# Performance work log

Measured on AMD Instinct MI355X. Metric: run time of the kernel, lower is better.

The kernel has to match this reference:

```python
import jax, jax.numpy as jnp
import numpy as np

N = 50000      # nodes
E = 800000     # edges
FIN = 128      # num_feature
EDIM = 16      # edge_dim
OUT = 64       # out_dim (per-head channels; concat=False averages heads)
H = 4          # heads
SCALE = 1.0 / float(np.sqrt(OUT))


def _layernorm(h, g, b):
    mu = h.mean(-1, keepdims=True)
    var = ((h - mu) ** 2).mean(-1, keepdims=True)
    return (h - mu) * jax.lax.rsqrt(var + 1e-5) * g + b


def _tconv(x, src, dst, ea, Wq, bq, Wk, bk, Wv, bv, We, Ws, bs):
    # PyG TransformerConv, concat=False, root_weight=True, eval mode (no dropout)
    n = x.shape[0]
    q = (x @ Wq + bq).reshape(n, H, OUT)[dst]   # [E,H,D] query at destination
    k = (x @ Wk + bk).reshape(n, H, OUT)[src]   # [E,H,D] key at source
    v = (x @ Wv + bv).reshape(n, H, OUT)[src]   # [E,H,D] value at source
    e = (ea @ We).reshape(-1, H, OUT)           # [E,H,D] edge embedding (no bias)
    logits = jnp.einsum('ehd,ehd->eh', q, k + e) * SCALE   # [E,H]
    # segment softmax over incoming edges of each destination node
    m = jax.lax.stop_gradient(jax.ops.segment_max(logits, dst, num_segments=n))
    a = jnp.exp(logits - m[dst])
    s = jax.ops.segment_sum(a, dst, num_segments=n)
    alpha = a / s[dst]                                     # [E,H]
    agg = jax.ops.segment_sum((v + e) * alpha[..., None], dst, num_segments=n)  # [N,H,D]
    return agg.mean(axis=1) + x @ Ws + bs      # concat=False -> head mean; + skip


def _forward(x, src, dst, ea, p1, p2, p3, g, b):
    h = x
    for p in (p1, p2, p3):
        h = jax.nn.gelu(_layernorm(_tconv(h, src, dst, ea, *p), g, b), approximate=False)
    return h


def setup_inputs() -> dict:
    key = jax.random.key(0)
    ks = iter(jax.random.split(key, 64))
    def nrm(shp, s=0.05):
        return jax.random.normal(next(ks), shp, jnp.float32) * s
    inp = {
        'x': nrm((N, FIN), 1.0),
        'edge_index': jax.random.randint(next(ks), (2, E), 0, N),
        'edge_attr': nrm((E, EDIM), 1.0),
    }
    for l, fin in ((1, FIN), (2, OUT), (3, OUT)):
        inp[f'Wq{l}'] = nrm((fin, H * OUT)); inp[f'bq{l}'] = jnp.zeros((H * OUT,), jnp.float32)
        inp[f'Wk{l}'] = nrm((fin, H * OUT)); inp[f'bk{l}'] = jnp.zeros((H * OUT,), jnp.float32)
        inp[f'Wv{l}'] = nrm((fin, H * OUT)); inp[f'bv{l}'] = jnp.zeros((H * OUT,), jnp.float32)
        inp[f'We{l}'] = nrm((EDIM, H * OUT))
        inp[f'Ws{l}'] = nrm((fin, OUT)); inp[f'bs{l}'] = jnp.zeros((OUT,), jnp.float32)
    inp['ln_g'] = jnp.ones((OUT,), jnp.float32)
    inp['ln_b'] = jnp.zeros((OUT,), jnp.float32)
    return inp


def reference(x, edge_index, edge_attr,
              Wq1, bq1, Wk1, bk1, Wv1, bv1, We1, Ws1, bs1,
              Wq2, bq2, Wk2, bk2, Wv2, bv2, We2, Ws2, bs2,
              Wq3, bq3, Wk3, bk3, Wv3, bv3, We3, Ws3, bs3,
              ln_g, ln_b):
    src, dst = edge_index[0], edge_index[1]
    p1 = (Wq1, bq1, Wk1, bk1, Wv1, bv1, We1, Ws1, bs1)
    p2 = (Wq2, bq2, Wk2, bk2, Wv2, bv2, We2, Ws2, bs2)
    p3 = (Wq3, bq3, Wk3, bk3, Wv3, bv3, We3, Ws3, bs3)
    return _forward(x, src, dst, edge_attr, p1, p2, p3, ln_g, ln_b)
```

## Files before the change

### kernel.cpp

```cpp
#include <hip/hip_runtime.h>
#include <hip/hip_bf16.h>
#include <math.h>

#define NNODES 50000
#define NEDGES 800000
#define HD     256
#define CW     448
#define NTOT   896
#define QS     0.18033688011112042f

typedef __hip_bfloat16 bf16;
typedef unsigned short u16;
typedef unsigned char  u8;
typedef unsigned int   u32;
typedef unsigned long long u64;
typedef __attribute__((ext_vector_type(8))) short bf16x8;
typedef __attribute__((ext_vector_type(4))) float f32x4;
typedef __attribute__((ext_vector_type(2))) float f32x2;

__device__ __forceinline__ float lo16f(u32 u) { return __uint_as_float(u << 16); }
__device__ __forceinline__ float hi16f(u32 u) { return __uint_as_float(u & 0xFFFF0000u); }
__device__ __forceinline__ short f2s(float v) { __hip_bfloat16 h = __float2bfloat16(v); return *(short*)&h; }

template<int CTRL>
__device__ __forceinline__ float dppadd(float x) {
    int t = __builtin_amdgcn_update_dpp(0, __float_as_int(x), CTRL, 0xF, 0xF, true);
    return x + __int_as_float(t);
}

__global__ void hist_kernel(const int* __restrict__ dst, int* __restrict__ deg, int E) {
    int e = blockIdx.x * 256 + threadIdx.x;
    if (e < E) atomicAdd(&deg[dst[e]], 1);
}

__global__ void scanA(const int* __restrict__ deg, int* __restrict__ locincl,
                      int* __restrict__ blocksum, int n) {
    int tid = threadIdx.x;
    int i = blockIdx.x * 256 + tid;
    int v = (i < n) ? deg[i] : 0;
    int lane = tid & 63, w = tid >> 6;
    int s = v;
    #pragma unroll
    for (int off = 1; off < 64; off <<= 1) {
        int t = __shfl_up(s, off);
        if (lane >= off) s += t;
    }
    __shared__ int wsum[4];
    if (lane == 63) wsum[w] = s;
    __syncthreads();
    for (int ww = 0; ww < w; ww++) s += wsum[ww];
    if (i < n) locincl[i] = s;
    if (tid == 255) blocksum[blockIdx.x] = s;
}

__global__ void scanB(const int* __restrict__ blocksum, int* __restrict__ blockoff,
                      int nb, int* __restrict__ rowptr, int n) {
    int tid = threadIdx.x;
    int v = (tid < nb) ? blocksum[tid] : 0;
    int lane = tid & 63, w = tid >> 6;
    int s = v;
    #pragma unroll
    for (int off = 1; off < 64; off <<= 1) {
        int t = __shfl_up(s, off);
        if (lane >= off) s += t;
    }
    __shared__ int wsum[4];
    if (lane == 63) wsum[w] = s;
    __syncthreads();
    for (int ww = 0; ww < w; ww++) s += wsum[ww];
    if (tid < nb) blockoff[tid] = s - v;
    if (tid == 255) rowptr[n] = s;
}

__global__ void scanC(const int* __restrict__ deg, const int* __restrict__ locincl,
                      const int* __restrict__ blockoff,
                      int* __restrict__ rowptr, int* __restrict__ cursor, int n) {
    int i = blockIdx.x * 256 + threadIdx.x;
    if (i < n) {
        int ex = locincl[i] - deg[i] + blockoff[blockIdx.x];
        rowptr[i] = ex;
        cursor[i] = ex;
    }
}

__global__ void scatter_kernel(const int* __restrict__ src, const int* __restrict__ dst,
                               int* __restrict__ cursor, int2* __restrict__ csr2, int E) {
    int e = blockIdx.x * 256 + threadIdx.x;
    if (e < E) {
        int d = dst[e];
        int p = atomicAdd(&cursor[d], 1);
        csr2[p] = make_int2(src[e], e);
    }
}

__global__ void pack_all(const float* __restrict__ Wq, const float* __restrict__ bq,
                         const float* __restrict__ Wk, const float* __restrict__ bk,
                         const float* __restrict__ Wv, const float* __restrict__ bv,
                         const float* __restrict__ We,
                         const float* __restrict__ Ws, const float* __restrict__ bs,
                         bf16* __restrict__ Wc, float* __restrict__ b, int K) {
    int n = blockIdx.x, c = threadIdx.x;
    float v, bb;
    if (n < 256)      { v = Wq[(size_t)c * 256 + n] * QS;    bb = bq[n] * QS; }
    else if (n < 320) {
        int t = n - 256, h = t >> 4, j = t & 15;
        float s = 0.f, sb = 0.f;
        #pragma unroll 8
        for (int d = 0; d < 64; d++) {
            float wv = We[j * HD + h * 64 + d];
            s += Wq[(size_t)c * 256 + h * 64 + d] * wv;
            sb += bq[h * 64 + d] * wv;
        }
        v = s * QS; bb = sb * QS;
    }
    else if (n < 384) { v = Ws[(size_t)c * 64  + (n - 320)]; bb = bs[n - 320]; }
    else if (n < 640) { v = Wv[(size_t)c * 256 + (n - 384)]; bb = bv[n - 384]; }
    else              { v = Wk[(size_t)c * 256 + (n - 640)]; bb = bk[n - 640]; }
    Wc[(size_t)n * K + c] = __float2bfloat16(v);
    if (c == 0) b[n] = bb;
}

template<typename TA, int K>
__global__ void __launch_bounds__(256) gemm_fused(
    const TA* __restrict__ A, const bf16* __restrict__ Wc, const float* __restrict__ bias,
    bf16* __restrict__ comb, bf16* __restrict__ vbuf, u8* __restrict__ k8)
{
    constexpr int KS  = K / 32;
    constexpr int CPR = K / 8;
    constexpr int SLD = CPR / 4;
    __shared__ short Bl[64 * K];
    __shared__ u8    Tr[64 * 128];
    int tid = threadIdx.x, w = tid >> 6, lane = tid & 63;
    int cl = lane & 15, aq = lane >> 4;
    int m0 = blockIdx.x * 64;
    int m  = m0 + w * 16 + cl;
    int rowc = (m < NNODES) ? m : (NNODES - 1);

    bf16x8 af[KS];
    if constexpr (sizeof(TA) == 4) {
        const float* ar = (const float*)A + (size_t)rowc * K;
        #pragma unroll
        for (int ks = 0; ks < KS; ks++) {
            const float4* ap = (const float4*)(ar + ks * 32 + aq * 8);
            float4 f0 = ap[0], f1 = ap[1];
            union { short s[8]; bf16x8 v; } t;
            t.s[0] = f2s(f0.x); t.s[1] = f2s(f0.y); t.s[2] = f2s(f0.z); t.s[3] = f2s(f0.w);
            t.s[4] = f2s(f1.x); t.s[5] = f2s(f1.y); t.s[6] = f2s(f1.z); t.s[7] = f2s(f1.w);
            af[ks] = t.v;
        }
    } else {
        const u16* ar = (const u16*)A + (size_t)rowc * K;
        #pragma unroll
        for (int ks = 0; ks < KS; ks++) af[ks] = *(const bf16x8*)(ar + ks * 32 + aq * 8);
    }

    uint4 sreg[SLD];
    auto SLOAD = [&](int chunk) {
        #pragma unroll
        for (int p = 0; p < SLD; p++) {
            int slot = tid + p * 256;
            int row = slot / CPR, j = slot % CPR;
            sreg[p] = *(const uint4*)((const u16*)Wc + (size_t)(chunk * 64 + row) * K + (j << 3));
        }
    };
    SLOAD(0);

    for (int chunk = 0; chunk < 14; chunk++) {
        __syncthreads();
        #pragma unroll
        for (int p = 0; p < SLD; p++) {
            int slot = tid + p * 256;
            int row = slot / CPR, j = slot % CPR;
            *(uint4*)&Bl[row * K + ((j ^ (row & 7)) << 3)] = sreg[p];
        }
        if (chunk < 13) SLOAD(chunk + 1);
        __syncthreads();

        f32x4 acc[4] = {};
        #pragma unroll
        for (int t = 0; t < 4; t++) {
            #pragma unroll
            for (int ks = 0; ks < KS; ks++) {
                int g = ((ks * 4 + aq) ^ (cl & 7)) << 3;
                bf16x8 bfr = *(const bf16x8*)&Bl[(t * 16 + cl) * K + g];
                acc[t] = __builtin_amdgcn_mfma_f32_16x16x32_bf16(bfr, af[ks], acc[t], 0, 0, 0);
            }
        }

        int r = w * 16 + cl;
        if (chunk < 10) {
            #pragma unroll
            for (int t = 0; t < 4; t++) {
                float4 bv = *(const float4*)&bias[chunk * 64 + t * 16 + aq * 4];
                u32 lo = (u32)(u16)f2s(acc[t][0] + bv.x) | ((u32)(u16)f2s(acc[t][1] + bv.y) << 16);
                u32 hi = (u32)(u16)f2s(acc[t][2] + bv.z) | ((u32)(u16)f2s(acc[t][3] + bv.w) << 16);
                *(uint2*)&Tr[r * 128 + (((t * 4 + aq) ^ (r & 15)) << 3)] = make_uint2(lo, hi);
            }
        } else {
            #pragma unroll
            for (int t = 0; t < 4; t++) {
                float4 bv = *(const float4*)&bias[chunk * 64 + t * 16 + aq * 4];
                u32 pk = __builtin_amdgcn_cvt_pk_fp8_f32(acc[t][0] + bv.x, acc[t][1] + bv.y, 0, false);
                pk = __builtin_amdgcn_cvt_pk_fp8_f32(acc[t][2] + bv.z, acc[t][3] + bv.w, pk, true);
                *(u32*)&Tr[r * 64 + (((t * 4 + aq) ^ (r & 15)) << 2)] = pk;
            }
        }
        __syncthreads();

        int r2 = tid >> 2, q = tid & 3;
        int gr = m0 + r2;
        if (gr < NNODES) {
            if (chunk < 10) {
                union { u32 d[4]; uint4 v; } o0, o1;
                #pragma unroll
                for (int j = 0; j < 4; j++) {
                    int g = ((q * 4 + j) ^ (r2 & 15)) << 3;
                    uint2 dv = *(const uint2*)&Tr[r2 * 128 + g];
                    if (j < 2) { o0.d[2 * j] = dv.x; o0.d[2 * j + 1] = dv.y; }
                    else       { o1.d[2 * (j - 2)] = dv.x; o1.d[2 * (j - 2) + 1] = dv.y; }
                }
                char* dst;
                if (chunk < 6) dst = (char*)comb + (size_t)gr * (CW * 2) + chunk * 128;
                else           dst = (char*)vbuf + (size_t)gr * 512 + (chunk - 6) * 128;
                *(uint4*)(dst + q * 32)      = o0.v;
                *(uint4*)(dst + q * 32 + 16) = o1.v;
            } else {
                union { u32 d[4]; uint4 v; } o;
                #pragma unroll
                for (int j = 0; j < 4; j++) {
                    int g = ((q * 4 + j) ^ (r2 & 15)) << 2;
                    o.d[j] = *(const u32*)&Tr[r2 * 64 + g];
                }
                *(uint4*)((char*)k8 + (size_t)gr * 256 + (chunk - 10) * 64 + q * 16) = o.v;
            }
        }
    }
}

__global__ void __launch_bounds__(256) node_fused(
    const int* __restrict__ rowptr, const int2* __restrict__ csr2,
    const float* __restrict__ eattr, const u16* __restrict__ comb,
    const u16* __restrict__ vbuf, const u8* __restrict__ k8,
    const float* __restrict__ We, const float* __restrict__ lng, const float* __restrict__ lnb,
    bf16* __restrict__ outB, float* __restrict__ outF)
{
    int tid = threadIdx.x, w = tid >> 6, lane = tid & 63;
    int n = blockIdx.x * 4 + w;
    int hg = lane >> 4, j16 = lane & 15, coff = 4 * lane;
    __shared__ float sAV[4][256];
    __shared__ float sAE[4][64];

    const u16* crow = comb + (size_t)n * CW;
    uint2 qv = *(const uint2*)(crow + coff);
    float qf0 = lo16f(qv.x), qf1 = hi16f(qv.x), qf2 = lo16f(qv.y), qf3 = hi16f(qv.y);
    float qwe_r = __uint_as_float((u32)crow[256 + lane] << 16);

    int e0 = __builtin_amdgcn_readfirstlane(rowptr[n]);
    int e1 = __builtin_amdgcn_readfirstlane(rowptr[n + 1]);

    float ss = 0.f, av0 = 0.f, av1 = 0.f, av2 = 0.f, av3 = 0.f, ae = 0.f;
    u32 vo = (u32)coff * 2u;
    u32 eo = (u32)j16 * 4u;

    auto EDGE = [&](int2 me) {
        u32 s = (u32)me.x, eid = (u32)me.y;
        u32   kw = *(const u32*)  ((const char*)k8    + ((s << 8) + (u32)coff));
        uint2 vw = *(const uint2*)((const char*)vbuf  + ((s << 9) + vo));
        float ea = *(const float*)((const char*)eattr + ((eid << 6) + eo));
        f32x2 k01 = __builtin_amdgcn_cvt_pk_f32_fp8(kw, false);
        f32x2 k23 = __builtin_amdgcn_cvt_pk_f32_fp8(kw, true);
        float part = qf0 * k01[0] + qf1 * k01[1] + qf2 * k23[0] + qf3 * k23[1] + qwe_r * ea;
        part = dppadd<0xB1>(part);
        part = dppadd<0x4E>(part);
        part = dppadd<0x141>(part);
        part = dppadd<0x140>(part);
        float alpha = __builtin_amdgcn_exp2f(part);
        ss += alpha;
        ae += alpha * ea;
        av0 += alpha * lo16f(vw.x); av1 += alpha * hi16f(vw.x);
        av2 += alpha * lo16f(vw.y); av3 += alpha * hi16f(vw.y);
    };

    int i = e0;
    int2 c0 = make_int2(0, 0), c1 = c0, c2 = c0, c3 = c0;
    if (i + 3 < e1) { c0 = csr2[i]; c1 = csr2[i + 1]; c2 = csr2[i + 2]; c3 = csr2[i + 3]; }
    for (; i + 7 < e1; i += 4) {
        int2 p0 = csr2[i + 4], p1 = csr2[i + 5], p2 = csr2[i + 6], p3 = csr2[i + 7];
        EDGE(c0); EDGE(c1); EDGE(c2); EDGE(c3);
        c0 = p0; c1 = p1; c2 = p2; c3 = p3;
    }
    if (i + 3 < e1) { EDGE(c0); EDGE(c1); EDGE(c2); EDGE(c3); i += 4; }
    for (; i < e1; ++i) { int2 cc = csr2[i]; EDGE(cc); }

    float inv = (ss > 0.f) ? 1.f / ss : 0.f;
    *(float4*)&sAV[w][coff] = make_float4(av0 * inv, av1 * inv, av2 * inv, av3 * inv);
    sAE[w][lane] = ae * inv;

    int d = lane;
    float val = 0.f;
    #pragma unroll
    for (int h = 0; h < 4; h++) {
        float xv = sAV[w][h * 64 + d];
        #pragma unroll
        for (int j = 0; j < 16; j++) xv += sAE[w][h * 16 + j] * We[j * HD + h * 64 + d];
        val += xv;
    }
    val = val * 0.25f + __uint_as_float((u32)crow[320 + d] << 16);

    float m = val;
    #pragma unroll
    for (int off = 1; off < 64; off <<= 1) m += __shfl_xor(m, off);
    m *= (1.f / 64.f);
    float diff = val - m;
    float vr = diff * diff;
    #pragma unroll
    for (int off = 1; off < 64; off <<= 1) vr += __shfl_xor(vr, off);
    vr *= (1.f / 64.f);
    float y = diff * rsqrtf(vr + 1e-5f) * lng[d] + lnb[d];
    float ge = 0.5f * y * (1.f + erff(y * 0.70710678118654752f));
    if (outF) outF[(size_t)n * 64 + d] = ge;
    else      outB[(size_t)n * 64 + d] = __float2bfloat16(ge);
}

extern "C" void kernel_launch(void* const* d_in, const int* in_sizes, int n_in,
                              void* d_out, int out_size, void* d_ws, size_t ws_size,
                              hipStream_t stream)
{
    const float* x     = (const float*)d_in[0];
    const int*   eidx  = (const int*)d_in[1];
    const float* eattr = (const float*)d_in[2];
    struct P { const float *Wq,*bq,*Wk,*bk,*Wv,*bv,*We,*Ws,*bs; };
    P p[3];
    for (int l = 0; l < 3; l++) {
        int base = 3 + l * 9;
        p[l].Wq = (const float*)d_in[base + 0]; p[l].bq = (const float*)d_in[base + 1];
        p[l].Wk = (const float*)d_in[base + 2]; p[l].bk = (const float*)d_in[base + 3];
        p[l].Wv = (const float*)d_in[base + 4]; p[l].bv = (const float*)d_in[base + 5];
        p[l].We = (const float*)d_in[base + 6];
        p[l].Ws = (const float*)d_in[base + 7]; p[l].bs = (const float*)d_in[base + 8];
    }
    const float* lng = (const float*)d_in[30];
    const float* lnb = (const float*)d_in[31];

    char* ws = (char*)d_ws;
    size_t off = 0;
    auto alloc = [&](size_t bytes) { void* pp = ws + off; off += (bytes + 255) & ~(size_t)255; return pp; };
    int*   rowptr   = (int*)  alloc((NNODES + 1) * 4);
    int*   cursor   = (int*)  alloc(NNODES * 4);
    int*   deg      = (int*)  alloc(NNODES * 4);
    int*   blocksum = (int*)  alloc(256 * 4);
    int*   blockoff = (int*)  alloc(256 * 4);
    int2*  csr2     = (int2*) alloc((size_t)NEDGES * 8);
    bf16*  hbuf     = (bf16*) alloc((size_t)NNODES * 64 * 2);
    bf16*  comb     = (bf16*) alloc((size_t)NNODES * CW * 2);
    bf16*  vbuf     = (bf16*) alloc((size_t)NNODES * 256 * 2);
    u8*    k8       = (u8*)   alloc((size_t)NNODES * 256);
    bf16*  Wc       = (bf16*) alloc((size_t)NTOT * 128 * 2);
    float* b896     = (float*)alloc(NTOT * 4);
    (void)ws_size;

    const int* srcArr = eidx;
    const int* dstArr = eidx + NEDGES;

    int NB = (NNODES + 255) / 256;
    (void)hipMemsetAsync(deg, 0, NNODES * 4, stream);
    hist_kernel<<<(NEDGES + 255) / 256, 256, 0, stream>>>(dstArr, deg, NEDGES);
    scanA<<<NB, 256, 0, stream>>>(deg, cursor, blocksum, NNODES);
    scanB<<<1, 256, 0, stream>>>(blocksum, blockoff, NB, rowptr, NNODES);
    scanC<<<NB, 256, 0, stream>>>(deg, cursor, blockoff, rowptr, cursor, NNODES);
    scatter_kernel<<<(NEDGES + 255) / 256, 256, 0, stream>>>(srcArr, dstArr, cursor, csr2, NEDGES);

    int gm = (NNODES + 63) / 64;
    int fins[3] = {128, 64, 64};

    const void* hin = x;
    for (int l = 0; l < 3; l++) {
        int FIN = fins[l];
        pack_all<<<NTOT, FIN, 0, stream>>>(p[l].Wq, p[l].bq, p[l].Wk, p[l].bk,
                                           p[l].Wv, p[l].bv, p[l].We, p[l].Ws, p[l].bs,
                                           Wc, b896, FIN);
        if (l == 0) gemm_fused<float, 128><<<gm, 256, 0, stream>>>((const float*)hin, Wc, b896, comb, vbuf, k8);
        else        gemm_fused<bf16,  64><<<gm, 256, 0, stream>>>((const bf16*)hin,  Wc, b896, comb, vbuf, k8);
        node_fused<<<NNODES / 4, 256, 0, stream>>>(rowptr, csr2, eattr, (const u16*)comb,
            (const u16*)vbuf, k8, p[l].We, lng, lnb,
            (l == 2) ? nullptr : hbuf, (l == 2) ? (float*)d_out : nullptr);
        hin = hbuf;
    }
}
```

Baseline: 733.4 us.

## Drop LDS staging in projection GEMM, split chunks over grid, scalarize edge addresses

The projection GEMM no longer stages weight tiles and output tiles through shared memory with barriers. Each wave now reads its B fragments straight from global memory (cache-resident weights) and writes results directly to the output buffers. The 14 output chunks are split across a second grid dimension to double the number of blocks, and the comb row stride shrinks from 448 to 384. In the edge loop, source and edge ids are made wave-uniform via readfirstlane so address arithmetic can stay scalar. The trade-off is fewer barriers and less LDS traffic against narrower, less coalesced global stores and repeated weight reads from cache.

```diff
diff --git a/kernel.cpp b/kernel.cpp
--- a/kernel.cpp
+++ b/kernel.cpp
@@ -5,7 +5,7 @@
 #define NNODES 50000
 #define NEDGES 800000
 #define HD     256
-#define CW     448
+#define CW     384
 #define NTOT   896
 #define QS     0.18033688011112042f
 
@@ -125,16 +125,12 @@
     const TA* __restrict__ A, const bf16* __restrict__ Wc, const float* __restrict__ bias,
     bf16* __restrict__ comb, bf16* __restrict__ vbuf, u8* __restrict__ k8)
 {
-    constexpr int KS  = K / 32;
-    constexpr int CPR = K / 8;
-    constexpr int SLD = CPR / 4;
-    __shared__ short Bl[64 * K];
-    __shared__ u8    Tr[64 * 128];
+    constexpr int KS = K / 32;
     int tid = threadIdx.x, w = tid >> 6, lane = tid & 63;
     int cl = lane & 15, aq = lane >> 4;
-    int m0 = blockIdx.x * 64;
-    int m  = m0 + w * 16 + cl;
+    int m = blockIdx.x * 64 + w * 16 + cl;
     int rowc = (m < NNODES) ? m : (NNODES - 1);
+    int cbeg = blockIdx.y * 7;
 
     bf16x8 af[KS];
     if constexpr (sizeof(TA) == 4) {
@@ -154,84 +150,38 @@
         for (int ks = 0; ks < KS; ks++) af[ks] = *(const bf16x8*)(ar + ks * 32 + aq * 8);
     }
 
-    uint4 sreg[SLD];
-    auto SLOAD = [&](int chunk) {
-        #pragma unroll
-        for (int p = 0; p < SLD; p++) {
-            int slot = tid + p * 256;
-            int row = slot / CPR, j = slot % CPR;
-            sreg[p] = *(const uint4*)((const u16*)Wc + (size_t)(chunk * 64 + row) * K + (j << 3));
-        }
-    };
-    SLOAD(0);
-
-    for (int chunk = 0; chunk < 14; chunk++) {
-        __syncthreads();
-        #pragma unroll
-        for (int p = 0; p < SLD; p++) {
-            int slot = tid + p * 256;
-            int row = slot / CPR, j = slot % CPR;
-            *(uint4*)&Bl[row * K + ((j ^ (row & 7)) << 3)] = sreg[p];
-        }
-        if (chunk < 13) SLOAD(chunk + 1);
-        __syncthreads();
-
+    for (int ci = 0; ci < 7; ci++) {
+        int chunk = cbeg + ci;
+        const u16* wbase = (const u16*)Wc + (size_t)chunk * 64 * K + (size_t)cl * K + aq * 8;
         f32x4 acc[4] = {};
         #pragma unroll
         for (int t = 0; t < 4; t++) {
             #pragma unroll
             for (int ks = 0; ks < KS; ks++) {
-                int g = ((ks * 4 + aq) ^ (cl & 7)) << 3;
-                bf16x8 bfr = *(const bf16x8*)&Bl[(t * 16 + cl) * K + g];
+                bf16x8 bfr = *(const bf16x8*)(wbase + (size_t)t * 16 * K + ks * 32);
                 acc[t] = __builtin_amdgcn_mfma_f32_16x16x32_bf16(bfr, af[ks], acc[t], 0, 0, 0);
             }
         }
-
-        int r = w * 16 + cl;
+        if (m >= NNODES) continue;
         if (chunk < 10) {
+            u16* dst;
+            if (chunk < 6) dst = (u16*)comb + (size_t)m * CW + chunk * 64;
+            else           dst = (u16*)vbuf + (size_t)m * 256 + (chunk - 6) * 64;
             #pragma unroll
             for (int t = 0; t < 4; t++) {
                 float4 bv = *(const float4*)&bias[chunk * 64 + t * 16 + aq * 4];
                 u32 lo = (u32)(u16)f2s(acc[t][0] + bv.x) | ((u32)(u16)f2s(acc[t][1] + bv.y) << 16);
                 u32 hi = (u32)(u16)f2s(acc[t][2] + bv.z) | ((u32)(u16)f2s(acc[t][3] + bv.w) << 16);
-                *(uint2*)&Tr[r * 128 + (((t * 4 + aq) ^ (r & 15)) << 3)] = make_uint2(lo, hi);
+                *(uint2*)(dst + t * 16 + aq * 4) = make_uint2(lo, hi);
             }
         } else {
+            u8* dst = k8 + (size_t)m * 256 + (chunk - 10) * 64;
             #pragma unroll
             for (int t = 0; t < 4; t++) {
                 float4 bv = *(const float4*)&bias[chunk * 64 + t * 16 + aq * 4];
                 u32 pk = __builtin_amdgcn_cvt_pk_fp8_f32(acc[t][0] + bv.x, acc[t][1] + bv.y, 0, false);
                 pk = __builtin_amdgcn_cvt_pk_fp8_f32(acc[t][2] + bv.z, acc[t][3] + bv.w, pk, true);
-                *(u32*)&Tr[r * 64 + (((t * 4 + aq) ^ (r & 15)) << 2)] = pk;
-            }
-        }
-        __syncthreads();
-
-        int r2 = tid >> 2, q = tid & 3;
-        int gr = m0 + r2;
-        if (gr < NNODES) {
-            if (chunk < 10) {
-                union { u32 d[4]; uint4 v; } o0, o1;
-                #pragma unroll
-                for (int j = 0; j < 4; j++) {
-                    int g = ((q * 4 + j) ^ (r2 & 15)) << 3;
-                    uint2 dv = *(const uint2*)&Tr[r2 * 128 + g];
-                    if (j < 2) { o0.d[2 * j] = dv.x; o0.d[2 * j + 1] = dv.y; }
-                    else       { o1.d[2 * (j - 2)] = dv.x; o1.d[2 * (j - 2) + 1] = dv.y; }
-                }
-                char* dst;
-                if (chunk < 6) dst = (char*)comb + (size_t)gr * (CW * 2) + chunk * 128;
-                else           dst = (char*)vbuf + (size_t)gr * 512 + (chunk - 6) * 128;
-                *(uint4*)(dst + q * 32)      = o0.v;
-                *(uint4*)(dst + q * 32 + 16) = o1.v;
-            } else {
-                union { u32 d[4]; uint4 v; } o;
-                #pragma unroll
-                for (int j = 0; j < 4; j++) {
-                    int g = ((q * 4 + j) ^ (r2 & 15)) << 2;
-                    o.d[j] = *(const u32*)&Tr[r2 * 64 + g];
-                }
-                *(uint4*)((char*)k8 + (size_t)gr * 256 + (chunk - 10) * 64 + q * 16) = o.v;
+                *(u32*)(dst + t * 16 + aq * 4) = pk;
             }
         }
     }
@@ -263,10 +213,14 @@
     u32 eo = (u32)j16 * 4u;
 
     auto EDGE = [&](int2 me) {
-        u32 s = (u32)me.x, eid = (u32)me.y;
-        u32   kw = *(const u32*)  ((const char*)k8    + ((s << 8) + (u32)coff));
-        uint2 vw = *(const uint2*)((const char*)vbuf  + ((s << 9) + vo));
-        float ea = *(const float*)((const char*)eattr + ((eid << 6) + eo));
+        u32 s   = (u32)__builtin_amdgcn_readfirstlane(me.x);
+        u32 eid = (u32)__builtin_amdgcn_readfirstlane(me.y);
+        const char* kp = (const char*)k8    + ((size_t)s << 8);
+        const char* vp = (const char*)vbuf  + ((size_t)s << 9);
+        const char* ep = (const char*)eattr + ((size_t)eid << 6);
+        u32   kw = *(const u32*)  (kp + coff);
+        uint2 vw = *(const uint2*)(vp + vo);
+        float ea = *(const float*)(ep + eo);
         f32x2 k01 = __builtin_amdgcn_cvt_pk_f32_fp8(kw, false);
         f32x2 k23 = __builtin_amdgcn_cvt_pk_f32_fp8(kw, true);
         float part = qf0 * k01[0] + qf1 * k01[1] + qf2 * k23[0] + qf3 * k23[1] + qwe_r * ea;
@@ -379,8 +333,8 @@
         pack_all<<<NTOT, FIN, 0, stream>>>(p[l].Wq, p[l].bq, p[l].Wk, p[l].bk,
                                            p[l].Wv, p[l].bv, p[l].We, p[l].Ws, p[l].bs,
                                            Wc, b896, FIN);
-        if (l == 0) gemm_fused<float, 128><<<gm, 256, 0, stream>>>((const float*)hin, Wc, b896, comb, vbuf, k8);
-        else        gemm_fused<bf16,  64><<<gm, 256, 0, stream>>>((const bf16*)hin,  Wc, b896, comb, vbuf, k8);
+        if (l == 0) gemm_fused<float, 128><<<dim3(gm, 2), 256, 0, stream>>>((const float*)hin, Wc, b896, comb, vbuf, k8);
+        else        gemm_fused<bf16,  64><<<dim3(gm, 2), 256, 0, stream>>>((const bf16*)hin,  Wc, b896, comb, vbuf, k8);
         node_fused<<<NNODES / 4, 256, 0, stream>>>(rowptr, csr2, eattr, (const u16*)comb,
             (const u16*)vbuf, k8, p[l].We, lng, lnb,
             (l == 2) ? nullptr : hbuf, (l == 2) ? (float*)d_out : nullptr);
```

New measurement: 788.3 us. 7.5% more time.
